# Optimization experiments

Hardware: AMD Instinct MI355X
Metric: run time of the kernel (lower is better)

The kernel has to match this reference:

```python
import jax, jax.numpy as jnp
import numpy as np

HIDDEN = 1024

def setup_inputs() -> dict:
    key = jax.random.key(0)
    ks = jax.random.split(key, 7)
    s = 1.0 / np.sqrt(HIDDEN)
    X = jax.random.normal(ks[0], (4, 2048, HIDDEN), dtype=jnp.float32)
    Wq = jax.random.uniform(ks[1], (HIDDEN, HIDDEN), jnp.float32, -s, s)
    bq = jax.random.uniform(ks[2], (HIDDEN,), jnp.float32, -s, s)
    Wk = jax.random.uniform(ks[3], (HIDDEN, HIDDEN), jnp.float32, -s, s)
    bk = jax.random.uniform(ks[4], (HIDDEN,), jnp.float32, -s, s)
    Wv = jax.random.uniform(ks[5], (HIDDEN, HIDDEN), jnp.float32, -s, s)
    bv = jax.random.uniform(ks[6], (HIDDEN,), jnp.float32, -s, s)
    return {"X": X, "Wq": Wq, "bq": bq, "Wk": Wk, "bk": bk, "Wv": Wv, "bv": bv}

def reference(X, Wq, bq, Wk, bk, Wv, bv):
    # torch Linear: x @ W.T + b
    q = jnp.einsum('bsd,ed->bse', X, Wq) + bq  # [B,S,H]
    k = jnp.einsum('bsd,ed->bse', X, Wk) + bk
    v = jnp.einsum('bsd,ed->bse', X, Wv) + bv
    scores = jnp.einsum('bqd,bkd->bqk', q, k) / jnp.sqrt(jnp.float32(HIDDEN))  # [B,S,S]
    attn = jax.nn.softmax(scores, axis=-1)
    return jnp.einsum('bqk,bkd->bqd', attn, v)
```

## Files before the change

### kernel.cpp

```cpp
#include <hip/hip_runtime.h>
#include <hip/hip_bf16.h>
#include <stdint.h>

#define B_ 4
#define S_ 2048
#define H_ 1024

typedef __attribute__((ext_vector_type(4))) float f32x4;
typedef __attribute__((ext_vector_type(8))) short bf16x8;

#define AS1C(p) ((const __attribute__((address_space(1))) void*)(p))
#define AS3(p)  ((__attribute__((address_space(3))) void*)(p))

__global__ __launch_bounds__(256)
void prep_k(const float* __restrict__ X,
            const float* __restrict__ Wq, const float* __restrict__ Wk,
            const float* __restrict__ Wv,
            const float* __restrict__ bq, const float* __restrict__ bk,
            const float* __restrict__ bv,
            __hip_bfloat16* __restrict__ Xb, __hip_bfloat16* __restrict__ Wall,
            float* __restrict__ ball, float* __restrict__ rsum)
{
    const int NX = B_ * S_ * H_ / 4;
    const int NW = H_ * H_ / 4;
    const int TOT = NX + 3 * NW + 3 * H_ / 4 + B_ * S_ / 4;
    const int stride = gridDim.x * blockDim.x;
    for (int i = blockIdx.x * blockDim.x + threadIdx.x; i < TOT; i += stride) {
        if (i < NX + 3 * NW) {
            const float* src; uint64_t* dst; int li;
            if (i < NX) { src = X; dst = (uint64_t*)Xb; li = i; }
            else {
                int j = i - NX;
                int wsel = j / NW; li = j - wsel * NW;
                src = (wsel == 0) ? Wq : (wsel == 1) ? Wk : Wv;
                dst = (uint64_t*)Wall + (size_t)wsel * NW;
            }
            float4 v = ((const float4*)src)[li];
            union { __hip_bfloat16 h[4]; uint64_t u; } o;
            o.h[0] = __float2bfloat16(v.x);
            o.h[1] = __float2bfloat16(v.y);
            o.h[2] = __float2bfloat16(v.z);
            o.h[3] = __float2bfloat16(v.w);
            dst[li] = o.u;
        } else {
            int j = i - (NX + 3 * NW);
            if (j < 3 * H_ / 4) {
                int bsel = j >> 8;
                int off  = j & 255;
                const float* src = (bsel == 0) ? bq : (bsel == 1) ? bk : bv;
                ((float4*)ball)[j] = ((const float4*)src)[off];
            } else {
                int j2 = j - 3 * H_ / 4;
                ((float4*)rsum)[j2] = make_float4(0.f, 0.f, 0.f, 0.f);
            }
        }
    }
}

template<int BN, int MINW, bool OUT_BF16, bool HAS_BIAS, bool V_SPLIT, bool EXP_SUM, bool ROWDIV>
__global__ __launch_bounds__(256, MINW)
void gemm_bt(const __hip_bfloat16* __restrict__ A, int lda, long long aBatch,
             const __hip_bfloat16* __restrict__ B, int ldb, long long bBatch,
             const float* __restrict__ bias,
             void* __restrict__ Cout, int ldc, long long cBatch,
             __hip_bfloat16* __restrict__ vtrans, float* __restrict__ rsum,
             int M, int N, int K, float scale)
{
    constexpr int FJ = BN / 32;
    constexpr int SN = BN / 32;
    __shared__ __hip_bfloat16 lA[128 * 64];
    __shared__ __hip_bfloat16 lB[BN * 64];

    const int t  = threadIdx.x;
    const int bz = blockIdx.z;
    A += (long long)bz * aBatch;
    B += (long long)bz * bBatch;
    const int bm = blockIdx.y * 128;
    const int bn = blockIdx.x * BN;

    const int wave = t >> 6;
    const int lane = t & 63;
    const int wm = (wave & 1) * 64;
    const int wn = (wave >> 1) * (BN / 2);
    const int lm = lane & 15;
    const int kq = lane >> 4;
    const int cro = lm & 7;

    f32x4 acc[4][FJ] = {};

    const int srow = t >> 3;
    const int swz  = ((t & 7) ^ ((t >> 3) & 7)) * 8;
    const __hip_bfloat16* gA = A + (long long)(bm + srow) * lda + swz;
    const __hip_bfloat16* gB = B + (long long)(bn + srow) * ldb + swz;
    __hip_bfloat16* sA = lA + t * 8;
    __hip_bfloat16* sB = lB + t * 8;

    for (int k0 = 0; k0 < K; k0 += 64) {
        __syncthreads();
#pragma unroll
        for (int s = 0; s < 4; ++s)
            __builtin_amdgcn_global_load_lds(AS1C(gA + (long long)s * 32 * lda + k0),
                                             AS3(sA + s * 2048), 16, 0, 0);
#pragma unroll
        for (int s = 0; s < SN; ++s)
            __builtin_amdgcn_global_load_lds(AS1C(gB + (long long)s * 32 * ldb + k0),
                                             AS3(sB + s * 2048), 16, 0, 0);
        __syncthreads();

#pragma unroll
        for (int ks = 0; ks < 2; ++ks) {
            bf16x8 af[4], bfr[FJ];
            const int ch = ((ks * 4 + kq) ^ cro) * 8;
#pragma unroll
            for (int i = 0; i < 4; ++i)
                af[i] = *(const bf16x8*)(lA + (wm + i * 16 + lm) * 64 + ch);
#pragma unroll
            for (int j = 0; j < FJ; ++j)
                bfr[j] = *(const bf16x8*)(lB + (wn + j * 16 + lm) * 64 + ch);
#pragma unroll
            for (int i = 0; i < 4; ++i)
#pragma unroll
                for (int j = 0; j < FJ; ++j)
                    acc[i][j] = __builtin_amdgcn_mfma_f32_16x16x32_bf16(af[i], bfr[j], acc[i][j], 0, 0, 0);
        }
    }

    const bool vmode = V_SPLIT && (bn >= 2 * H_);
    const int r0q = kq * 4;

    if (EXP_SUM) {
#pragma unroll
        for (int i = 0; i < 4; ++i) {
            const int rowb = bm + wm + i * 16 + r0q;
            float ps[4] = {0.f, 0.f, 0.f, 0.f};
#pragma unroll
            for (int j = 0; j < FJ; ++j) {
                const int col = bn + wn + j * 16 + lm;
#pragma unroll
                for (int r = 0; r < 4; ++r) {
                    float e = __expf(acc[i][j][r] * scale);
                    ps[r] += e;
                    ((__hip_bfloat16*)Cout)[(long long)bz * cBatch +
                        (long long)(rowb + r) * ldc + col] = __float2bfloat16(e);
                }
            }
#pragma unroll
            for (int r = 0; r < 4; ++r) {
#pragma unroll
                for (int m = 1; m < 16; m <<= 1)
                    ps[r] += __shfl_xor(ps[r], m);
            }
            if (lm == 0) {
#pragma unroll
                for (int r = 0; r < 4; ++r)
                    atomicAdd(rsum + bz * S_ + rowb + r, ps[r]);
            }
        }
        return;
    }

#pragma unroll
    for (int i = 0; i < 4; ++i) {
        const int rowb = bm + wm + i * 16 + r0q;
        float inv[4];
        if (ROWDIV) {
            float4 rs = *(const float4*)(rsum + bz * S_ + rowb);
            inv[0] = 1.0f / rs.x; inv[1] = 1.0f / rs.y;
            inv[2] = 1.0f / rs.z; inv[3] = 1.0f / rs.w;
        }
#pragma unroll
        for (int j = 0; j < FJ; ++j) {
            const int col = bn + wn + j * 16 + lm;
            float bvv = 0.0f;
            if (HAS_BIAS) bvv = bias[col];
            if (!vmode) {
#pragma unroll
                for (int r = 0; r < 4; ++r) {
                    float val = ROWDIV ? acc[i][j][r] * inv[r]
                                       : acc[i][j][r] * scale + bvv;
                    long long idx = (long long)bz * cBatch + (long long)(rowb + r) * ldc + col;
                    if (OUT_BF16) ((__hip_bfloat16*)Cout)[idx] = __float2bfloat16(val);
                    else          ((float*)Cout)[idx] = val;
                }
            } else {
                const long long ebase = (long long)((rowb >> 11) * H_ + col - 2 * H_) * S_;
                union { ushort4 u; __hip_bfloat16 h[4]; } o;
#pragma unroll
                for (int r = 0; r < 4; ++r)
                    o.h[r] = __float2bfloat16(acc[i][j][r] + bvv);
                *(ushort4*)(vtrans + ebase + (rowb & 2047)) = o.u;
            }
        }
    }
}

extern "C" void kernel_launch(void* const* d_in, const int* in_sizes, int n_in,
                              void* d_out, int out_size, void* d_ws, size_t ws_size,
                              hipStream_t stream)
{
    const float* X  = (const float*)d_in[0];
    const float* Wq = (const float*)d_in[1];
    const float* bq = (const float*)d_in[2];
    const float* Wk = (const float*)d_in[3];
    const float* bk = (const float*)d_in[4];
    const float* Wv = (const float*)d_in[5];
    const float* bv = (const float*)d_in[6];
    float* out = (float*)d_out;

    char* w = (char*)d_ws;
    const size_t MB = 1ull << 20;
    __hip_bfloat16* Xb   = (__hip_bfloat16*)(w + 0);
    __hip_bfloat16* Wall = (__hip_bfloat16*)(w + 16 * MB);
    float*          ball = (float*)        (w + 22 * MB);
    __hip_bfloat16* sc   = (__hip_bfloat16*)(w + 0);
    __hip_bfloat16* qk   = (__hip_bfloat16*)(w + 32 * MB);
    __hip_bfloat16* vtb  = (__hip_bfloat16*)(w + 64 * MB);
    float*          rsum = (float*)        (w + 80 * MB);

    prep_k<<<2048, 256, 0, stream>>>(X, Wq, Wk, Wv, bq, bk, bv,
                                     Xb, Wall, ball, rsum);

    dim3 g1(3 * H_ / 128, (B_ * S_) / 128, 1);
    gemm_bt<128, 1, true, true, true, false, false><<<g1, 256, 0, stream>>>(
        Xb, H_, 0, Wall, H_, 0, ball, qk, 2 * H_, 0, vtb, nullptr,
        B_ * S_, 3 * H_, H_, 1.0f);

    dim3 g2(S_ / 128, S_ / 128, B_);
    gemm_bt<128, 4, true, false, false, true, false><<<g2, 256, 0, stream>>>(
        qk,      2 * H_, (long long)S_ * 2 * H_,
        qk + H_, 2 * H_, (long long)S_ * 2 * H_,
        nullptr, sc, S_, (long long)S_ * S_, nullptr, rsum, S_, S_, H_, 0.03125f);

    dim3 g3(H_ / 128, S_ / 128, B_);
    gemm_bt<128, 4, false, false, false, false, true><<<g3, 256, 0, stream>>>(
        sc,  S_, (long long)S_ * S_,
        vtb, S_, (long long)H_ * S_,
        nullptr, out, H_, (long long)S_ * H_, nullptr, rsum, S_, H_, S_, 1.0f);
}
```

Before: 247.8 us.

## Triple-buffer LDS with async prefetch and 256x128 tiles in GEMM kernels

Replaces the single-buffered 128x128 GEMM with a 512-thread, 256x128-tile kernel that keeps three LDS stages in flight. Global-to-LDS loads for tile k+3 are issued while computing tile k, and explicit vmcnt waits and barriers replace the load-then-sync loop. The goal is to hide global memory latency and raise per-block compute reuse. In exchange it uses about 144KB of LDS, limiting occupancy to one block per CU, and gives fewer blocks per grid.

```diff
diff --git a/kernel.cpp b/kernel.cpp
--- a/kernel.cpp
+++ b/kernel.cpp
@@ -11,6 +11,9 @@
 
 #define AS1C(p) ((const __attribute__((address_space(1))) void*)(p))
 #define AS3(p)  ((__attribute__((address_space(3))) void*)(p))
+#define BAR()     __builtin_amdgcn_s_barrier()
+#define SCHED0()  __builtin_amdgcn_sched_barrier(0)
+#define WAITVM(n) asm volatile("s_waitcnt vmcnt(" #n ")" ::: "memory")
 
 __global__ __launch_bounds__(256)
 void prep_k(const float* __restrict__ X,
@@ -57,71 +60,94 @@
     }
 }
 
-template<int BN, int MINW, bool OUT_BF16, bool HAS_BIAS, bool V_SPLIT, bool EXP_SUM, bool ROWDIV>
-__global__ __launch_bounds__(256, MINW)
-void gemm_bt(const __hip_bfloat16* __restrict__ A, int lda, long long aBatch,
-             const __hip_bfloat16* __restrict__ B, int ldb, long long bBatch,
-             const float* __restrict__ bias,
-             void* __restrict__ Cout, int ldc, long long cBatch,
-             __hip_bfloat16* __restrict__ vtrans, float* __restrict__ rsum,
-             int M, int N, int K, float scale)
+template<bool OUT_BF16, bool HAS_BIAS, bool V_SPLIT, bool EXP_SUM, bool ROWDIV>
+__global__ __launch_bounds__(512, 1)
+void gemm3r(const __hip_bfloat16* __restrict__ A, int lda, long long aBatch,
+            const __hip_bfloat16* __restrict__ B, int ldb, long long bBatch,
+            const float* __restrict__ bias,
+            void* __restrict__ Cout, int ldc, long long cBatch,
+            __hip_bfloat16* __restrict__ vtrans, float* __restrict__ rsum,
+            int K, float scale)
 {
-    constexpr int FJ = BN / 32;
-    constexpr int SN = BN / 32;
-    __shared__ __hip_bfloat16 lA[128 * 64];
-    __shared__ __hip_bfloat16 lB[BN * 64];
+    __shared__ __hip_bfloat16 lA[3][256 * 64];
+    __shared__ __hip_bfloat16 lB[3][128 * 64];
 
     const int t  = threadIdx.x;
     const int bz = blockIdx.z;
     A += (long long)bz * aBatch;
     B += (long long)bz * bBatch;
-    const int bm = blockIdx.y * 128;
-    const int bn = blockIdx.x * BN;
+    const int bm = blockIdx.y * 256;
+    const int bn = blockIdx.x * 128;
 
     const int wave = t >> 6;
     const int lane = t & 63;
-    const int wm = (wave & 1) * 64;
-    const int wn = (wave >> 1) * (BN / 2);
+    const int wm = (wave >> 1) * 64;
+    const int wn = (wave & 1) * 64;
     const int lm = lane & 15;
     const int kq = lane >> 4;
     const int cro = lm & 7;
 
-    f32x4 acc[4][FJ] = {};
+    f32x4 acc[4][4] = {};
 
     const int srow = t >> 3;
-    const int swz  = ((t & 7) ^ ((t >> 3) & 7)) * 8;
+    const int swz  = ((t & 7) ^ (srow & 7)) * 8;
     const __hip_bfloat16* gA = A + (long long)(bm + srow) * lda + swz;
     const __hip_bfloat16* gB = B + (long long)(bn + srow) * ldb + swz;
-    __hip_bfloat16* sA = lA + t * 8;
-    __hip_bfloat16* sB = lB + t * 8;
-
-    for (int k0 = 0; k0 < K; k0 += 64) {
-        __syncthreads();
-#pragma unroll
-        for (int s = 0; s < 4; ++s)
-            __builtin_amdgcn_global_load_lds(AS1C(gA + (long long)s * 32 * lda + k0),
-                                             AS3(sA + s * 2048), 16, 0, 0);
-#pragma unroll
-        for (int s = 0; s < SN; ++s)
-            __builtin_amdgcn_global_load_lds(AS1C(gB + (long long)s * 32 * ldb + k0),
-                                             AS3(sB + s * 2048), 16, 0, 0);
-        __syncthreads();
-
+
+    auto stage = [&](int s, int k0) {
+        __hip_bfloat16* dA = lA[s] + t * 8;
+        __hip_bfloat16* dB = lB[s] + t * 8;
+#pragma unroll
+        for (int g = 0; g < 4; ++g)
+            __builtin_amdgcn_global_load_lds(AS1C(gA + (long long)g * 64 * lda + k0),
+                                             AS3(dA + g * 4096), 16, 0, 0);
+#pragma unroll
+        for (int g = 0; g < 2; ++g)
+            __builtin_amdgcn_global_load_lds(AS1C(gB + (long long)g * 64 * ldb + k0),
+                                             AS3(dB + g * 4096), 16, 0, 0);
+    };
+
+    stage(0, 0); stage(1, 64); stage(2, 128);
+    SCHED0();
+    WAITVM(12);
+    SCHED0();
+    BAR();
+    SCHED0();
+
+    const int nT = K >> 6;
+    int sl = 0;
+    for (int tt = 0; tt < nT; ++tt) {
+        const __hip_bfloat16* cA = lA[sl] + (wm + lm) * 64;
+        const __hip_bfloat16* cB = lB[sl] + (wn + lm) * 64;
 #pragma unroll
         for (int ks = 0; ks < 2; ++ks) {
-            bf16x8 af[4], bfr[FJ];
             const int ch = ((ks * 4 + kq) ^ cro) * 8;
+            bf16x8 af[4], bfr[4];
 #pragma unroll
             for (int i = 0; i < 4; ++i)
-                af[i] = *(const bf16x8*)(lA + (wm + i * 16 + lm) * 64 + ch);
-#pragma unroll
-            for (int j = 0; j < FJ; ++j)
-                bfr[j] = *(const bf16x8*)(lB + (wn + j * 16 + lm) * 64 + ch);
+                af[i] = *(const bf16x8*)(cA + i * 16 * 64 + ch);
+#pragma unroll
+            for (int j = 0; j < 4; ++j)
+                bfr[j] = *(const bf16x8*)(cB + j * 16 * 64 + ch);
 #pragma unroll
             for (int i = 0; i < 4; ++i)
 #pragma unroll
-                for (int j = 0; j < FJ; ++j)
-                    acc[i][j] = __builtin_amdgcn_mfma_f32_16x16x32_bf16(af[i], bfr[j], acc[i][j], 0, 0, 0);
+                for (int j = 0; j < 4; ++j)
+                    acc[i][j] = __builtin_amdgcn_mfma_f32_16x16x32_bf16(
+                        af[i], bfr[j], acc[i][j], 0, 0, 0);
+        }
+        if (tt + 1 < nT) {
+            BAR();
+            SCHED0();
+            if (tt + 3 < nT) stage(sl, (tt + 3) * 64);
+            SCHED0();
+            if (tt + 3 < nT)      { WAITVM(12); }
+            else if (tt + 2 < nT) { WAITVM(6);  }
+            else                  { WAITVM(0);  }
+            SCHED0();
+            BAR();
+            SCHED0();
+            sl = (sl == 2) ? 0 : sl + 1;
         }
     }
 
@@ -134,7 +160,7 @@
             const int rowb = bm + wm + i * 16 + r0q;
             float ps[4] = {0.f, 0.f, 0.f, 0.f};
 #pragma unroll
-            for (int j = 0; j < FJ; ++j) {
+            for (int j = 0; j < 4; ++j) {
                 const int col = bn + wn + j * 16 + lm;
 #pragma unroll
                 for (int r = 0; r < 4; ++r) {
@@ -169,7 +195,7 @@
             inv[2] = 1.0f / rs.z; inv[3] = 1.0f / rs.w;
         }
 #pragma unroll
-        for (int j = 0; j < FJ; ++j) {
+        for (int j = 0; j < 4; ++j) {
             const int col = bn + wn + j * 16 + lm;
             float bvv = 0.0f;
             if (HAS_BIAS) bvv = bias[col];
@@ -220,20 +246,19 @@
     prep_k<<<2048, 256, 0, stream>>>(X, Wq, Wk, Wv, bq, bk, bv,
                                      Xb, Wall, ball, rsum);
 
-    dim3 g1(3 * H_ / 128, (B_ * S_) / 128, 1);
-    gemm_bt<128, 1, true, true, true, false, false><<<g1, 256, 0, stream>>>(
-        Xb, H_, 0, Wall, H_, 0, ball, qk, 2 * H_, 0, vtb, nullptr,
-        B_ * S_, 3 * H_, H_, 1.0f);
-
-    dim3 g2(S_ / 128, S_ / 128, B_);
-    gemm_bt<128, 4, true, false, false, true, false><<<g2, 256, 0, stream>>>(
+    dim3 g1(3 * H_ / 128, (B_ * S_) / 256, 1);
+    gemm3r<true, true, true, false, false><<<g1, 512, 0, stream>>>(
+        Xb, H_, 0, Wall, H_, 0, ball, qk, 2 * H_, 0, vtb, nullptr, H_, 1.0f);
+
+    dim3 g2(S_ / 128, S_ / 256, B_);
+    gemm3r<true, false, false, true, false><<<g2, 512, 0, stream>>>(
         qk,      2 * H_, (long long)S_ * 2 * H_,
         qk + H_, 2 * H_, (long long)S_ * 2 * H_,
-        nullptr, sc, S_, (long long)S_ * S_, nullptr, rsum, S_, S_, H_, 0.03125f);
-
-    dim3 g3(H_ / 128, S_ / 128, B_);
-    gemm_bt<128, 4, false, false, false, false, true><<<g3, 256, 0, stream>>>(
+        nullptr, sc, S_, (long long)S_ * S_, nullptr, rsum, H_, 0.03125f);
+
+    dim3 g3(H_ / 128, S_ / 256, B_);
+    gemm3r<false, false, false, false, true><<<g3, 512, 0, stream>>>(
         sc,  S_, (long long)S_ * S_,
         vtb, S_, (long long)H_ * S_,
-        nullptr, out, H_, (long long)S_ * H_, nullptr, rsum, S_, H_, S_, 1.0f);
+        nullptr, out, H_, (long long)S_ * H_, nullptr, rsum, S_, 1.0f);
 }
```

Measured after the change: 276.2 us. 1.11x slower.
